# Kernel tuning notes

Measured on AMD Instinct MI355X. Metric: run time of the kernel, lower is better.

The kernel has to match this reference:

```python
import jax, jax.numpy as jnp
import numpy as np

D_MODEL = 1024
NH_KD = 1024
RANK = 16
ALPHA = 1.0
SCALING = ALPHA / RANK


def setup_inputs() -> dict:
    key = jax.random.key(0)
    ks = jax.random.split(key, 7)
    std = 1.0 / np.sqrt(D_MODEL)
    x = jax.random.normal(ks[0], (4, 4096, D_MODEL), dtype=jnp.float32)
    # torch nn.Linear weight layout: [out, in]
    w_qkv = jax.random.normal(ks[1], (3 * NH_KD, D_MODEL), dtype=jnp.float32) * std
    b_qkv = jax.random.normal(ks[2], (3 * NH_KD,), dtype=jnp.float32) * 0.01
    a_q = jax.random.normal(ks[3], (RANK, D_MODEL), dtype=jnp.float32) * std
    b_q = jnp.zeros((NH_KD, RANK), dtype=jnp.float32) + jax.random.normal(ks[4], (NH_KD, RANK), dtype=jnp.float32) * 0.02
    a_v = jax.random.normal(ks[5], (RANK, D_MODEL), dtype=jnp.float32) * std
    b_v = jnp.zeros((NH_KD, RANK), dtype=jnp.float32) + jax.random.normal(ks[6], (NH_KD, RANK), dtype=jnp.float32) * 0.02
    return {"x": x, "w_qkv": w_qkv, "b_qkv": b_qkv, "a_q": a_q, "b_q": b_q, "a_v": a_v, "b_v": b_v}


def reference(x, w_qkv, b_qkv, a_q, b_q, a_v, b_v):
    # base QKV: [B,S,D] x [3*nh_kd, D]^T -> [B,S,3*nh_kd]
    qkv = jnp.einsum('bsd,od->bso', x, w_qkv) + b_qkv
    q = qkv[..., :NH_KD]
    k = qkv[..., NH_KD:2 * NH_KD]
    v = qkv[..., 2 * NH_KD:]
    # LoRA: x @ a^T @ b^T, scaled
    q = q + jnp.einsum('bsr,or->bso', jnp.einsum('bsd,rd->bsr', x, a_q), b_q) * SCALING
    v = v + jnp.einsum('bsr,or->bso', jnp.einsum('bsd,rd->bsr', x, a_v), b_v) * SCALING
    return jnp.concatenate([q, k, v], axis=-1)
```

## Files before the change

kernel.cpp:

```cpp
#include <hip/hip_runtime.h>

typedef unsigned int u32;
typedef unsigned short u16;
typedef short s16x8 __attribute__((ext_vector_type(8)));
typedef u16 u16x8 __attribute__((ext_vector_type(8)));
typedef float f32x4 __attribute__((ext_vector_type(4)));
typedef __attribute__((address_space(3))) u32 as3_u32;
typedef __attribute__((address_space(1))) const u32 as1_u32;

constexpr int MM = 16384, NN = 3072, KK = 1024;
constexpr int BM = 128, BN = 128, BK = 64;

__device__ __forceinline__ u16 f2bf(float f) {
  u32 u = __builtin_bit_cast(u32, f);
  u = (u + 0x7FFFu + ((u >> 16) & 1u)) >> 16;
  return (u16)u;
}

__device__ __forceinline__ void gload_lds16(const void* g, void* l) {
  __builtin_amdgcn_global_load_lds((as1_u32*)g, (as3_u32*)l, 16, 0, 0);
}

__global__ __launch_bounds__(256) void build_weff(
    const float* __restrict__ w, const float* __restrict__ aq,
    const float* __restrict__ bq, const float* __restrict__ av,
    const float* __restrict__ bv, u16* __restrict__ weff) {
  int idx = blockIdx.x * 256 + threadIdx.x;
  int o = idx >> 10, d = idx & 1023;
  float val = w[idx];
  if (o < 1024) {
    float s = 0.f;
#pragma unroll
    for (int r = 0; r < 16; ++r) s += bq[o * 16 + r] * aq[r * 1024 + d];
    val += s * 0.0625f;
  } else if (o >= 2048) {
    int o2 = o - 2048;
    float s = 0.f;
#pragma unroll
    for (int r = 0; r < 16; ++r) s += bv[o2 * 16 + r] * av[r * 1024 + d];
    val += s * 0.0625f;
  }
  weff[idx] = f2bf(val);
}

__global__ __launch_bounds__(256) void cvt_x(const float* __restrict__ x,
                                             u16* __restrict__ xb) {
  size_t i = ((size_t)blockIdx.x * 256 + threadIdx.x) * 8;
  float4 f0 = *(const float4*)(x + i);
  float4 f1 = *(const float4*)(x + i + 4);
  u16x8 o;
  o[0] = f2bf(f0.x); o[1] = f2bf(f0.y); o[2] = f2bf(f0.z); o[3] = f2bf(f0.w);
  o[4] = f2bf(f1.x); o[5] = f2bf(f1.y); o[6] = f2bf(f1.z); o[7] = f2bf(f1.w);
  *(u16x8*)(xb + i) = o;
}

template <bool REGA>
__global__ __launch_bounds__(256) void gemm_qkv(
    const u16* __restrict__ Ab, const float* __restrict__ Af,
    const u16* __restrict__ Bw, const float* __restrict__ bias,
    float* __restrict__ C) {
  __shared__ u16 As[BM * BK];
  __shared__ u16 Bs[BN * BK];
  const int tid = threadIdx.x;
  const int wave = tid >> 6, lane = tid & 63;
  const int l15 = lane & 15, lk = lane >> 4;
  const int mTile = blockIdx.y * BM, nTile = blockIdx.x * BN;
  const int wr = wave >> 1, wc = wave & 1;

  f32x4 acc[4][4] = {};

  for (int k0 = 0; k0 < KK; k0 += BK) {
#pragma unroll
    for (int j = 0; j < 4; ++j) {
      const int c = wave * 4 + j;
      const int e = c * 512 + lane * 8;
      const int row = e >> 6, col = e & 63;
      gload_lds16(Bw + (size_t)(nTile + row) * KK + k0 + col, Bs + c * 512);
    }
    if constexpr (!REGA) {
#pragma unroll
      for (int j = 0; j < 4; ++j) {
        const int c = wave * 4 + j;
        const int e = c * 512 + lane * 8;
        const int row = e >> 6, col = e & 63;
        gload_lds16(Ab + (size_t)(mTile + row) * KK + k0 + col, As + c * 512);
      }
    } else {
#pragma unroll
      for (int j = 0; j < 4; ++j) {
        const int e = (j * 256 + tid) * 8;
        const int row = e >> 6, col = e & 63;
        const float* g = Af + (size_t)(mTile + row) * KK + k0 + col;
        float4 f0 = *(const float4*)g;
        float4 f1 = *(const float4*)(g + 4);
        u16x8 o;
        o[0] = f2bf(f0.x); o[1] = f2bf(f0.y); o[2] = f2bf(f0.z); o[3] = f2bf(f0.w);
        o[4] = f2bf(f1.x); o[5] = f2bf(f1.y); o[6] = f2bf(f1.z); o[7] = f2bf(f1.w);
        *(u16x8*)(As + e) = o;
      }
    }
    __syncthreads();

    s16x8 af[4][2], bf[4][2];
#pragma unroll
    for (int m = 0; m < 4; ++m)
#pragma unroll
      for (int t = 0; t < 2; ++t)
        af[m][t] = *(const s16x8*)(As + (wr * 64 + m * 16 + l15) * BK + t * 32 + lk * 8);
#pragma unroll
    for (int n = 0; n < 4; ++n)
#pragma unroll
      for (int t = 0; t < 2; ++t)
        bf[n][t] = *(const s16x8*)(Bs + (wc * 64 + n * 16 + l15) * BK + t * 32 + lk * 8);

#pragma unroll
    for (int t = 0; t < 2; ++t)
#pragma unroll
      for (int m = 0; m < 4; ++m)
#pragma unroll
        for (int n = 0; n < 4; ++n)
          acc[m][n] = __builtin_amdgcn_mfma_f32_16x16x32_bf16(af[m][t], bf[n][t],
                                                              acc[m][n], 0, 0, 0);
    __syncthreads();
  }

  const int row0 = mTile + wr * 64, col0 = nTile + wc * 64;
#pragma unroll
  for (int n = 0; n < 4; ++n) {
    const int col = col0 + n * 16 + l15;
    const float bv = bias[col];
#pragma unroll
    for (int m = 0; m < 4; ++m) {
      const int r0 = row0 + m * 16 + lk * 4;
#pragma unroll
      for (int j = 0; j < 4; ++j)
        C[(size_t)(r0 + j) * NN + col] = acc[m][n][j] + bv;
    }
  }
}

extern "C" void kernel_launch(void* const* d_in, const int* in_sizes, int n_in,
                              void* d_out, int out_size, void* d_ws, size_t ws_size,
                              hipStream_t stream) {
  const float* x     = (const float*)d_in[0];
  const float* w_qkv = (const float*)d_in[1];
  const float* b_qkv = (const float*)d_in[2];
  const float* a_q   = (const float*)d_in[3];
  const float* b_q   = (const float*)d_in[4];
  const float* a_v   = (const float*)d_in[5];
  const float* b_v   = (const float*)d_in[6];
  float* out = (float*)d_out;

  u16* weff = (u16*)d_ws;
  const size_t weff_elems = (size_t)NN * KK;
  u16* xb = weff + weff_elems;
  const size_t need = (weff_elems + (size_t)MM * KK) * sizeof(u16);

  build_weff<<<dim3(NN * KK / 256), dim3(256), 0, stream>>>(w_qkv, a_q, b_q,
                                                            a_v, b_v, weff);
  if (ws_size >= need) {
    cvt_x<<<dim3(MM * KK / 8 / 256), dim3(256), 0, stream>>>(x, xb);
    gemm_qkv<false><<<dim3(NN / BN, MM / BM), dim3(256), 0, stream>>>(
        xb, nullptr, weff, b_qkv, out);
  } else {
    gemm_qkv<true><<<dim3(NN / BN, MM / BM), dim3(256), 0, stream>>>(
        nullptr, x, weff, b_qkv, out);
  }
}
```

Before: 187.2 us.

## Replace QKV GEMM with 256x256 double-buffered 8-wave pipelined MFMA kernel

The main bf16 GEMM moves from 128x128 tiles with 4 waves to 256x256 tiles with 8 waves. LDS is double-buffered and XOR-swizzled, and the global-to-LDS loads for the next k-step are interleaved with MFMA quarters under fine-grained barriers and vmcnt waits. It also adds an XCD-aware block remap and raises s_setprio around the MFMA bursts. The aim is to hide load latency, raise data reuse per tile and cut LDS bank conflicts. In exchange it uses more LDS and registers per block, and only 768 blocks are launched, which may leave some CUs idle in the tail.

```diff
diff --git a/kernel.cpp b/kernel.cpp
--- a/kernel.cpp
+++ b/kernel.cpp
@@ -9,7 +9,10 @@
 typedef __attribute__((address_space(1))) const u32 as1_u32;
 
 constexpr int MM = 16384, NN = 3072, KK = 1024;
-constexpr int BM = 128, BN = 128, BK = 64;
+constexpr int BM = 256, BN = 256, BK = 64;
+constexpr int NT = KK / BK;
+
+template <int V> struct IC { static constexpr int value = V; };
 
 __device__ __forceinline__ u16 f2bf(float f) {
   u32 u = __builtin_bit_cast(u32, f);
@@ -54,22 +57,148 @@
   *(u16x8*)(xb + i) = o;
 }
 
-template <bool REGA>
-__global__ __launch_bounds__(256) void gemm_qkv(
-    const u16* __restrict__ Ab, const float* __restrict__ Af,
-    const u16* __restrict__ Bw, const float* __restrict__ bias,
-    float* __restrict__ C) {
-  __shared__ u16 As[BM * BK];
-  __shared__ u16 Bs[BN * BK];
+__global__ __launch_bounds__(512, 2) void gemm8p(
+    const u16* __restrict__ Ag, const u16* __restrict__ Bg,
+    const float* __restrict__ bias, float* __restrict__ C) {
+  __shared__ __align__(16) u16 sA[2][BM * BK];
+  __shared__ __align__(16) u16 sB[2][BN * BK];
+
   const int tid = threadIdx.x;
   const int wave = tid >> 6, lane = tid & 63;
+  const int wrow = wave >> 2, wcol = wave & 3;
   const int l15 = lane & 15, lk = lane >> 4;
-  const int mTile = blockIdx.y * BM, nTile = blockIdx.x * BN;
+  const int swz = (l15 & 7) << 4;
+  const int ko0 = ((lk * 16) ^ swz) >> 1;
+  const int ko1 = ((64 + lk * 16) ^ swz) >> 1;
+  const int sRow = lane >> 3;
+  const int sCol = ((lane & 7) ^ (lane >> 3)) << 3;
+
+  constexpr int NWG = (MM / BM) * (NN / BN);
+  const int b = blockIdx.x;
+  const int bs = (b & 7) * (NWG >> 3) + (b >> 3);
+  const int tileM = (bs / (NN / BN)) * BM;
+  const int tileN = (bs % (NN / BN)) * BN;
+
+  const u16* Agb = Ag + (size_t)tileM * KK;
+  const u16* Bgb = Bg + (size_t)tileN * KK;
+
+  f32x4 acc[8][4] = {};
+  s16x8 a[4][2], bl[2][2], bh[2][2];
+
+  auto STAGE = [&](const u16* __restrict__ G, int rowHalf, u16* ldsHalf, int kc) {
+#pragma unroll
+    for (int j = 0; j < 2; ++j) {
+      const int c = wave * 2 + j;
+      gload_lds16(G + (size_t)(rowHalf + c * 8 + sRow) * KK + kc + sCol,
+                  ldsHalf + c * 512);
+    }
+  };
+  auto LDA = [&](const u16* At, int mh) {
+#pragma unroll
+    for (int i = 0; i < 4; ++i) {
+      const int row = wrow * 128 + (mh * 4 + i) * 16 + l15;
+      const u16* p = At + row * 64;
+      a[i][0] = *(const s16x8*)(p + ko0);
+      a[i][1] = *(const s16x8*)(p + ko1);
+    }
+  };
+  auto LDB = [&](s16x8 (&bf)[2][2], const u16* Bt, int nh) {
+#pragma unroll
+    for (int i = 0; i < 2; ++i) {
+      const int row = wcol * 64 + (nh * 2 + i) * 16 + l15;
+      const u16* p = Bt + row * 64;
+      bf[i][0] = *(const s16x8*)(p + ko0);
+      bf[i][1] = *(const s16x8*)(p + ko1);
+    }
+  };
+  auto MFMA16 = [&](auto MH, auto NH, s16x8 (&bf)[2][2]) {
+    constexpr int mh = decltype(MH)::value, nh = decltype(NH)::value;
+    __builtin_amdgcn_s_setprio(1);
+#pragma unroll
+    for (int k2 = 0; k2 < 2; ++k2)
+#pragma unroll
+      for (int i = 0; i < 4; ++i)
+#pragma unroll
+        for (int j = 0; j < 2; ++j)
+          acc[mh * 4 + i][nh * 2 + j] = __builtin_amdgcn_mfma_f32_16x16x32_bf16(
+              a[i][k2], bf[j][k2], acc[mh * 4 + i][nh * 2 + j], 0, 0, 0);
+    __builtin_amdgcn_s_setprio(0);
+  };
+  auto BAR = [] {
+    asm volatile("" ::: "memory");
+    __builtin_amdgcn_s_barrier();
+    asm volatile("" ::: "memory");
+  };
+
+  auto KT = [&](int cb, int k1, int k2, int s1, int s2, int vm) {
+    const u16* Ac = sA[cb]; const u16* Bc = sB[cb];
+    LDA(Ac, 0); LDB(bl, Bc, 0);
+    if (s1) STAGE(Agb, 0, sA[cb ^ 1], k1);
+    BAR();
+    MFMA16(IC<0>{}, IC<0>{}, bl);
+    BAR();
+    LDB(bh, Bc, 1);
+    if (s1) STAGE(Agb, 128, sA[cb ^ 1] + 8192, k1);
+    BAR();
+    MFMA16(IC<0>{}, IC<1>{}, bh);
+    BAR();
+    LDA(Ac, 1);
+    if (s2) STAGE(Bgb, 0, sB[cb], k2);
+    BAR();
+    MFMA16(IC<1>{}, IC<1>{}, bh);
+    BAR();
+    if (s2) STAGE(Bgb, 128, sB[cb] + 8192, k2);
+    BAR();
+    MFMA16(IC<1>{}, IC<0>{}, bl);
+    if (vm == 4) asm volatile("s_waitcnt vmcnt(4)" ::: "memory");
+    else if (vm == 0) asm volatile("s_waitcnt vmcnt(0)" ::: "memory");
+    BAR();
+  };
+
+  STAGE(Agb, 0,   sA[0], 0);
+  STAGE(Agb, 128, sA[0] + 8192, 0);
+  STAGE(Bgb, 0,   sB[0], 0);
+  STAGE(Bgb, 128, sB[0] + 8192, 0);
+  STAGE(Bgb, 0,   sB[1], BK);
+  STAGE(Bgb, 128, sB[1] + 8192, BK);
+  asm volatile("s_waitcnt vmcnt(4)" ::: "memory");
+  BAR();
+
+#pragma unroll 1
+  for (int t = 0; t < NT - 2; t += 2) {
+    KT(0, (t + 1) * BK, (t + 2) * BK, 1, 1, 4);
+    KT(1, (t + 2) * BK, (t + 3) * BK, 1, 1, 4);
+  }
+  KT(0, (NT - 1) * BK, 0, 1, 0, 0);
+  KT(1, 0, 0, 0, 0, -1);
+
+  const int r0 = tileM + wrow * 128, c0 = tileN + wcol * 64;
+#pragma unroll
+  for (int n = 0; n < 4; ++n) {
+    const int col = c0 + n * 16 + l15;
+    const float bv = bias[col];
+#pragma unroll
+    for (int m = 0; m < 8; ++m) {
+      const int rr = r0 + m * 16 + lk * 4;
+#pragma unroll
+      for (int j = 0; j < 4; ++j)
+        C[(size_t)(rr + j) * NN + col] = acc[m][n][j] + bv;
+    }
+  }
+}
+
+__global__ __launch_bounds__(256) void gemm_fb(
+    const float* __restrict__ Af, const u16* __restrict__ Bw,
+    const float* __restrict__ bias, float* __restrict__ C) {
+  __shared__ u16 As[128 * 64];
+  __shared__ u16 Bs[128 * 64];
+  const int tid = threadIdx.x;
+  const int wave = tid >> 6, lane = tid & 63;
+  const int l15 = lane & 15, lkq = lane >> 4;
+  const int mTile = blockIdx.y * 128, nTile = blockIdx.x * 128;
   const int wr = wave >> 1, wc = wave & 1;
-
   f32x4 acc[4][4] = {};
-
-  for (int k0 = 0; k0 < KK; k0 += BK) {
+  for (int k0 = 0; k0 < KK; k0 += 64) {
 #pragma unroll
     for (int j = 0; j < 4; ++j) {
       const int c = wave * 4 + j;
@@ -77,42 +206,30 @@
       const int row = e >> 6, col = e & 63;
       gload_lds16(Bw + (size_t)(nTile + row) * KK + k0 + col, Bs + c * 512);
     }
-    if constexpr (!REGA) {
-#pragma unroll
-      for (int j = 0; j < 4; ++j) {
-        const int c = wave * 4 + j;
-        const int e = c * 512 + lane * 8;
-        const int row = e >> 6, col = e & 63;
-        gload_lds16(Ab + (size_t)(mTile + row) * KK + k0 + col, As + c * 512);
-      }
-    } else {
-#pragma unroll
-      for (int j = 0; j < 4; ++j) {
-        const int e = (j * 256 + tid) * 8;
-        const int row = e >> 6, col = e & 63;
-        const float* g = Af + (size_t)(mTile + row) * KK + k0 + col;
-        float4 f0 = *(const float4*)g;
-        float4 f1 = *(const float4*)(g + 4);
-        u16x8 o;
-        o[0] = f2bf(f0.x); o[1] = f2bf(f0.y); o[2] = f2bf(f0.z); o[3] = f2bf(f0.w);
-        o[4] = f2bf(f1.x); o[5] = f2bf(f1.y); o[6] = f2bf(f1.z); o[7] = f2bf(f1.w);
-        *(u16x8*)(As + e) = o;
-      }
+#pragma unroll
+    for (int j = 0; j < 4; ++j) {
+      const int e = (j * 256 + tid) * 8;
+      const int row = e >> 6, col = e & 63;
+      const float* g = Af + (size_t)(mTile + row) * KK + k0 + col;
+      float4 f0 = *(const float4*)g;
+      float4 f1 = *(const float4*)(g + 4);
+      u16x8 o;
+      o[0] = f2bf(f0.x); o[1] = f2bf(f0.y); o[2] = f2bf(f0.z); o[3] = f2bf(f0.w);
+      o[4] = f2bf(f1.x); o[5] = f2bf(f1.y); o[6] = f2bf(f1.z); o[7] = f2bf(f1.w);
+      *(u16x8*)(As + e) = o;
     }
     __syncthreads();
-
     s16x8 af[4][2], bf[4][2];
 #pragma unroll
     for (int m = 0; m < 4; ++m)
 #pragma unroll
       for (int t = 0; t < 2; ++t)
-        af[m][t] = *(const s16x8*)(As + (wr * 64 + m * 16 + l15) * BK + t * 32 + lk * 8);
+        af[m][t] = *(const s16x8*)(As + (wr * 64 + m * 16 + l15) * 64 + t * 32 + lkq * 8);
 #pragma unroll
     for (int n = 0; n < 4; ++n)
 #pragma unroll
       for (int t = 0; t < 2; ++t)
-        bf[n][t] = *(const s16x8*)(Bs + (wc * 64 + n * 16 + l15) * BK + t * 32 + lk * 8);
-
+        bf[n][t] = *(const s16x8*)(Bs + (wc * 64 + n * 16 + l15) * 64 + t * 32 + lkq * 8);
 #pragma unroll
     for (int t = 0; t < 2; ++t)
 #pragma unroll
@@ -123,7 +240,6 @@
                                                               acc[m][n], 0, 0, 0);
     __syncthreads();
   }
-
   const int row0 = mTile + wr * 64, col0 = nTile + wc * 64;
 #pragma unroll
   for (int n = 0; n < 4; ++n) {
@@ -131,10 +247,10 @@
     const float bv = bias[col];
 #pragma unroll
     for (int m = 0; m < 4; ++m) {
-      const int r0 = row0 + m * 16 + lk * 4;
+      const int rr = row0 + m * 16 + lkq * 4;
 #pragma unroll
       for (int j = 0; j < 4; ++j)
-        C[(size_t)(r0 + j) * NN + col] = acc[m][n][j] + bv;
+        C[(size_t)(rr + j) * NN + col] = acc[m][n][j] + bv;
     }
   }
 }
@@ -160,10 +276,10 @@
                                                             a_v, b_v, weff);
   if (ws_size >= need) {
     cvt_x<<<dim3(MM * KK / 8 / 256), dim3(256), 0, stream>>>(x, xb);
-    gemm_qkv<false><<<dim3(NN / BN, MM / BM), dim3(256), 0, stream>>>(
-        xb, nullptr, weff, b_qkv, out);
+    gemm8p<<<dim3((MM / BM) * (NN / BN)), dim3(512), 0, stream>>>(xb, weff,
+                                                                  b_qkv, out);
   } else {
-    gemm_qkv<true><<<dim3(NN / BN, MM / BM), dim3(256), 0, stream>>>(
-        nullptr, x, weff, b_qkv, out);
-  }
-}
+    gemm_fb<<<dim3(NN / 128, MM / 128), dim3(256), 0, stream>>>(x, weff,
+                                                                b_qkv, out);
+  }
+}
```

Result: faster. 155.4 us (-17.0%).
